# Kernel tuning notes

Measured on AMD Instinct MI355X. Metric: run time of the kernel, lower is better.

The kernel has to match this reference:

```python
import jax, jax.numpy as jnp
import numpy as np

N = 100000      # nodes
E = 3200000     # edges
IN_DIM = 128
HID = 128
OUT_DIM = 1
LAYERS = 8
ALPHA = 0.1
THETA = 0.5


def setup_inputs() -> dict:
    key = jax.random.key(0)
    ks = jax.random.split(key, 8)
    x = jax.random.normal(ks[0], (N, IN_DIM), dtype=jnp.float32)
    edge_index = jax.random.randint(ks[1], (2, E), 0, N, dtype=jnp.int64)
    edge_weight = jax.random.uniform(ks[2], (E,), dtype=jnp.float32)  # unused by original forward path
    W_in = jax.random.normal(ks[3], (IN_DIM, HID), dtype=jnp.float32) * 0.05
    b_in = jnp.zeros((HID,), dtype=jnp.float32)
    W_gcn = jax.random.normal(ks[4], (LAYERS, HID, HID), dtype=jnp.float32) * 0.05
    W_out = jax.random.normal(ks[5], (HID, OUT_DIM), dtype=jnp.float32) * 0.05
    b_out = jnp.zeros((OUT_DIM,), dtype=jnp.float32)
    return {"x": x, "edge_weight": edge_weight, "W_in": W_in, "b_in": b_in,
            "W_gcn": W_gcn, "W_out": W_out, "b_out": b_out, "edge_index": edge_index}


def _gcn_norm(edge_index, dtype):
    # add self loops (fill value 1), symmetric normalization deg^-1/2 A deg^-1/2
    sl = jnp.arange(N, dtype=edge_index.dtype)
    row = jnp.concatenate([edge_index[0], sl])
    col = jnp.concatenate([edge_index[1], sl])
    w = jnp.ones(row.shape[0], dtype=dtype)
    deg = jax.ops.segment_sum(w, col, num_segments=N)
    dinv = jnp.where(deg > 0, jax.lax.rsqrt(deg), 0.0)
    norm = dinv[row] * dinv[col]
    return row, col, norm


def reference(x, edge_weight, W_in, b_in, W_gcn, W_out, b_out, edge_index):
    row, col, norm = _gcn_norm(edge_index, x.dtype)
    h = x @ W_in + b_in            # initial_proj
    h0 = h                          # residual x0
    for i in range(LAYERS):
        # dropout is identity in eval mode
        msg = h[row] * norm[:, None]                       # gather + scale [E+N, HID]
        agg = jax.ops.segment_sum(msg, col, num_segments=N)
        s = (1.0 - ALPHA) * agg + ALPHA * h0               # identity-mapped residual
        beta = float(np.log(THETA / (i + 1) + 1.0))
        h = (1.0 - beta) * s + beta * (s @ W_gcn[i])       # GCNII weight mix
        h = jax.nn.relu(h)
    return h @ W_out + b_out
```

## Files before the change

### kernel.cpp

```cpp
#include <hip/hip_runtime.h>
#include <hip/hip_bf16.h>
#include <math.h>

#define N_NODES 100000
#define N_EDGES 3200000
#define HID 128
#define LAYERS 8
#define ALPHA 0.1f
#define THETA 0.5f

#define NBKT 391
#define BKT_STRIDE 10240
#define EPT 16
#define CHUNK 4096

typedef unsigned int uint;
typedef unsigned short ushort;
typedef __attribute__((ext_vector_type(8))) short short8;
typedef __attribute__((ext_vector_type(4))) float f32x4;

__device__ inline float bf_lo(uint p) { return __uint_as_float(p << 16); }
__device__ inline float bf_hi(uint p) { return __uint_as_float(p & 0xffff0000u); }
__device__ inline uint bf_pack(float x, float y) {
    uint ux = __float_as_uint(x), uy = __float_as_uint(y);
    uint rx = (ux + 0x7fffu + ((ux >> 16) & 1u)) >> 16;
    uint ry = (uy + 0x7fffu + ((uy >> 16) & 1u)) >> 16;
    return rx | (ry << 16);
}
__device__ inline ushort bfr(float x) {
    uint u = __float_as_uint(x);
    return (ushort)((u + 0x7fffu + ((u >> 16) & 1u)) >> 16);
}
__device__ inline float bff(ushort s) { return __uint_as_float(((uint)s) << 16); }

__global__ __launch_bounds__(256) void k_bucket(const int* __restrict__ rowi,
                                                const int* __restrict__ coli,
                                                uint* __restrict__ eb,
                                                int* __restrict__ gcnt) {
    __shared__ int bcnt[NBKT];
    __shared__ int gbase[NBKT];
    int t = threadIdx.x;
    for (int i = t; i < NBKT; i += 256) bcnt[i] = 0;
    __syncthreads();

    int e0 = blockIdx.x * CHUNK;
    int bk[EPT];
    int rk[EPT];
    uint rec[EPT];
#pragma unroll
    for (int j = 0; j < EPT; ++j) {
        int e = e0 + j * 256 + t;
        if (e < N_EDGES) {
            int r = rowi[e];
            int c = coli[e];
            bk[j] = c >> 8;
            rec[j] = ((uint)r << 8) | (uint)(c & 255);
            rk[j] = atomicAdd(&bcnt[bk[j]], 1);
        } else {
            bk[j] = -1;
        }
    }
    __syncthreads();
    for (int i = t; i < NBKT; i += 256) {
        int n = bcnt[i];
        gbase[i] = n ? atomicAdd(&gcnt[i], n) : 0;
    }
    __syncthreads();
#pragma unroll
    for (int j = 0; j < EPT; ++j) {
        if (bk[j] >= 0)
            eb[(size_t)bk[j] * BKT_STRIDE + gbase[bk[j]] + rk[j]] = rec[j];
    }
}

__global__ __launch_bounds__(512) void k_bscan(const int* __restrict__ gcnt,
                                               int* __restrict__ bbase) {
    __shared__ int lds[512];
    int t = threadIdx.x;
    int v = (t < NBKT) ? gcnt[t] : 0;
    lds[t] = v;
    __syncthreads();
    for (int off = 1; off < 512; off <<= 1) {
        int u = (t >= off) ? lds[t - off] : 0;
        __syncthreads();
        lds[t] += u;
        __syncthreads();
    }
    if (t < NBKT) bbase[t] = lds[t] - v;
}

__global__ __launch_bounds__(256) void k_node_ipt(const uint* __restrict__ eb,
                                                  const int* __restrict__ gcnt,
                                                  const int* __restrict__ bbase,
                                                  float* __restrict__ dinv,
                                                  int* __restrict__ indptr) {
    __shared__ int ncnt[256];
    __shared__ int sc[256];
    int b = blockIdx.x;
    int t = threadIdx.x;
    ncnt[t] = 0;
    __syncthreads();
    int ne = gcnt[b];
    const uint* ebp = eb + (size_t)b * BKT_STRIDE;
    for (int i = t; i < ne; i += 256) atomicAdd(&ncnt[ebp[i] & 255], 1);
    __syncthreads();
    int v = ncnt[t];
    sc[t] = v;
    __syncthreads();
    for (int off = 1; off < 256; off <<= 1) {
        int u = (t >= off) ? sc[t - off] : 0;
        __syncthreads();
        sc[t] += u;
        __syncthreads();
    }
    int node = b * 256 + t;
    if (node < N_NODES) {
        dinv[node] = rsqrtf((float)(v + 1));
        indptr[node] = bbase[b] + (sc[t] - v);
    }
    if (b == NBKT - 1 && t == 255) indptr[N_NODES] = N_EDGES;
}

__global__ __launch_bounds__(256) void k_fill2(const uint* __restrict__ eb,
                                               const int* __restrict__ gcnt,
                                               const float* __restrict__ dinv,
                                               const int* __restrict__ indptr,
                                               int2* __restrict__ csr) {
    __shared__ float sdv[256];
    __shared__ int scur[256];
    __shared__ int sipt[256];
    int b = blockIdx.x;
    int t = threadIdx.x;
    int node = b * 256 + t;
    sdv[t] = (node < N_NODES) ? dinv[node] : 0.f;
    sipt[t] = (node < N_NODES) ? indptr[node] : 0;
    scur[t] = 0;
    __syncthreads();
    int ne = gcnt[b];
    const uint* ebp = eb + (size_t)b * BKT_STRIDE;
    for (int i = t; i < ne; i += 256) {
        uint rec = ebp[i];
        int lc = rec & 255;
        int r = (int)(rec >> 8);
        int pos = sipt[lc] + atomicAdd(&scur[lc], 1);
        csr[pos] = make_int2(r, __float_as_int(dinv[r] * sdv[lc]));
    }
}

__global__ __launch_bounds__(256) void k_wprep(const float* __restrict__ Wg,
                                               ushort* __restrict__ Wt) {
    int l = blockIdx.x;
    const float* W = Wg + (size_t)l * HID * HID;
    ushort* T = Wt + (size_t)l * HID * HID;
    int t = threadIdx.x;
#pragma unroll
    for (int i = 0; i < 16; ++i) {
        int idx = t + 256 * i;
        int k = idx >> 5;
        int c4 = idx & 31;
        float4 v = *(const float4*)(W + (size_t)k * HID + c4 * 4);
        T[(c4 * 4 + 0) * HID + k] = bfr(v.x);
        T[(c4 * 4 + 1) * HID + k] = bfr(v.y);
        T[(c4 * 4 + 2) * HID + k] = bfr(v.z);
        T[(c4 * 4 + 3) * HID + k] = bfr(v.w);
    }
}

__global__ __launch_bounds__(256) void k_spmm(const uint* __restrict__ h,
                                              const uint* __restrict__ h0,
                                              const float* __restrict__ dinv,
                                              const int* __restrict__ indptr,
                                              const int2* __restrict__ csr,
                                              uint* __restrict__ s_out) {
    int node = blockIdx.x * 4 + (threadIdx.x >> 6);
    if (node >= N_NODES) return;
    int lane = threadIdx.x & 63;
    int beg = indptr[node];
    int end = indptr[node + 1];
    float di = dinv[node];
    uint hs = h[node * 64 + lane];
    uint h0v = h0[node * 64 + lane];
    float ax[8], ay[8];
#pragma unroll
    for (int j = 0; j < 8; ++j) { ax[j] = 0.f; ay[j] = 0.f; }
    int e = beg;
    for (; e + 16 <= end; e += 16) {
        int2 rr[16];
#pragma unroll
        for (int j = 0; j < 16; ++j) rr[j] = csr[e + j];
        uint p[16];
#pragma unroll
        for (int j = 0; j < 16; ++j) p[j] = h[rr[j].x * 64 + lane];
#pragma unroll
        for (int j = 0; j < 16; ++j) {
            float w = __int_as_float(rr[j].y);
            ax[j & 7] = fmaf(w, bf_lo(p[j]), ax[j & 7]);
            ay[j & 7] = fmaf(w, bf_hi(p[j]), ay[j & 7]);
        }
    }
    for (; e < end; e += 4) {
        int2 rr[4];
        float w[4];
#pragma unroll
        for (int j = 0; j < 4; ++j) {
            int idx = e + j;
            rr[j] = csr[idx < end ? idx : beg];
            w[j] = (idx < end) ? __int_as_float(rr[j].y) : 0.f;
        }
        uint p[4];
#pragma unroll
        for (int j = 0; j < 4; ++j) p[j] = h[rr[j].x * 64 + lane];
#pragma unroll
        for (int j = 0; j < 4; ++j) {
            ax[j] = fmaf(w[j], bf_lo(p[j]), ax[j]);
            ay[j] = fmaf(w[j], bf_hi(p[j]), ay[j]);
        }
    }
    float sum0 = ((ax[0] + ax[1]) + (ax[2] + ax[3])) + ((ax[4] + ax[5]) + (ax[6] + ax[7]));
    float sum1 = ((ay[0] + ay[1]) + (ay[2] + ay[3])) + ((ay[4] + ay[5]) + (ay[6] + ay[7]));
    float selfw = di * di;
    float rx = (1.0f - ALPHA) * fmaf(selfw, bf_lo(hs), sum0) + ALPHA * bf_lo(h0v);
    float ry = (1.0f - ALPHA) * fmaf(selfw, bf_hi(hs), sum1) + ALPHA * bf_hi(h0v);
    s_out[node * 64 + lane] = bf_pack(rx, ry);
}

__global__ __launch_bounds__(256) void k_gemm_in(const float* __restrict__ A,
                                                 const float* __restrict__ W,
                                                 const float* __restrict__ bias,
                                                 uint* __restrict__ out0,
                                                 uint* __restrict__ out1) {
    __shared__ float sT[32 * 64];
    __shared__ float Ws[32 * 128];
    int t = threadIdx.x;
    int tr = t & 15;
    int tc = t >> 4;
    int rowBase = blockIdx.x * 64;
    float acc[4][8] = {};

    for (int ko = 0; ko < HID; ko += 32) {
#pragma unroll
        for (int pass = 0; pass < 2; ++pass) {
            int lin = t + 256 * pass;
            int r = lin >> 3;
            int kq = lin & 7;
            int ar = rowBase + r;
            if (ar >= N_NODES) ar = N_NODES - 1;
            float4 v = *(const float4*)(A + (size_t)ar * HID + ko + 4 * kq);
            sT[(4 * kq + 0) * 64 + r] = v.x;
            sT[(4 * kq + 1) * 64 + r] = v.y;
            sT[(4 * kq + 2) * 64 + r] = v.z;
            sT[(4 * kq + 3) * 64 + r] = v.w;
        }
#pragma unroll
        for (int pass = 0; pass < 4; ++pass) {
            int lin = t + 256 * pass;
            int k = lin >> 5;
            int c4 = lin & 31;
            *(float4*)&Ws[k * 128 + 4 * c4] =
                *(const float4*)(W + (size_t)(ko + k) * HID + 4 * c4);
        }
        __syncthreads();
#pragma unroll
        for (int k = 0; k < 32; ++k) {
            float4 a = *(const float4*)&sT[k * 64 + 4 * tr];
            float4 w0 = *(const float4*)&Ws[k * 128 + 8 * tc];
            float4 w1 = *(const float4*)&Ws[k * 128 + 8 * tc + 4];
            float av[4] = {a.x, a.y, a.z, a.w};
            float wv[8] = {w0.x, w0.y, w0.z, w0.w, w1.x, w1.y, w1.z, w1.w};
#pragma unroll
            for (int i = 0; i < 4; ++i)
#pragma unroll
                for (int j = 0; j < 8; ++j)
                    acc[i][j] = fmaf(av[i], wv[j], acc[i][j]);
        }
        __syncthreads();
    }

    int c0 = 8 * tc;
    float bb[8];
#pragma unroll
    for (int j = 0; j < 8; ++j) bb[j] = bias[c0 + j];
#pragma unroll
    for (int i = 0; i < 4; ++i) {
        int r = rowBase + 4 * tr + i;
        if (r >= N_NODES) break;
        float v[8];
#pragma unroll
        for (int j = 0; j < 8; ++j) v[j] = acc[i][j] + bb[j];
        uint4 o;
        o.x = bf_pack(v[0], v[1]);
        o.y = bf_pack(v[2], v[3]);
        o.z = bf_pack(v[4], v[5]);
        o.w = bf_pack(v[6], v[7]);
        *(uint4*)(out0 + (size_t)r * 64 + c0 / 2) = o;
        *(uint4*)(out1 + (size_t)r * 64 + c0 / 2) = o;
    }
}

#define SAS 136

__global__ __launch_bounds__(256) void k_gemm_layer(const uint* __restrict__ A,
                                                    const ushort* __restrict__ Wt,
                                                    uint* __restrict__ out0,
                                                    float beta) {
    __shared__ ushort sA[64 * SAS];
    __shared__ ushort sW[128 * SAS];
    int t = threadIdx.x;
    int lane = t & 63;
    int wv = t >> 6;
    int rowBase = blockIdx.x * 64;

#pragma unroll
    for (int i = 0; i < 4; ++i) {
        int idx = t + 256 * i;
        int r = idx >> 4;
        int q = idx & 15;
        int ar = rowBase + r;
        if (ar >= N_NODES) ar = N_NODES - 1;
        uint4 v = *(const uint4*)(A + (size_t)ar * 64 + q * 4);
        *(uint4*)((uint*)(sA + r * SAS) + q * 4) = v;
    }
#pragma unroll
    for (int i = 0; i < 8; ++i) {
        int idx = t + 256 * i;
        int r = idx >> 4;
        int q = idx & 15;
        uint4 v = *(const uint4*)((const uint*)(Wt + (size_t)r * HID) + q * 4);
        *(uint4*)((uint*)(sW + r * SAS) + q * 4) = v;
    }
    __syncthreads();

    int fr = lane & 15;
    int fq = lane >> 4;
    f32x4 acc[4][2] = {};
#pragma unroll
    for (int kc = 0; kc < 4; ++kc) {
        int kof = kc * 32 + fq * 8;
        short8 b0 = *(const short8*)(sW + (wv * 32 + fr) * SAS + kof);
        short8 b1 = *(const short8*)(sW + (wv * 32 + 16 + fr) * SAS + kof);
#pragma unroll
        for (int tm = 0; tm < 4; ++tm) {
            short8 a = *(const short8*)(sA + (tm * 16 + fr) * SAS + kof);
            acc[tm][0] = __builtin_amdgcn_mfma_f32_16x16x32_bf16(a, b0, acc[tm][0], 0, 0, 0);
            acc[tm][1] = __builtin_amdgcn_mfma_f32_16x16x32_bf16(a, b1, acc[tm][1], 0, 0, 0);
        }
    }
    __syncthreads();

    ushort* pack = sW;
    float ob = 1.0f - beta;
#pragma unroll
    for (int tm = 0; tm < 4; ++tm)
#pragma unroll
        for (int tn = 0; tn < 2; ++tn)
#pragma unroll
            for (int r = 0; r < 4; ++r) {
                int row = tm * 16 + fq * 4 + r;
                int col = wv * 32 + tn * 16 + fr;
                float sv = bff(sA[row * SAS + col]);
                float val = fmaxf(fmaf(ob, sv, beta * acc[tm][tn][r]), 0.f);
                pack[row * 128 + col] = bfr(val);
            }
    __syncthreads();
#pragma unroll
    for (int i = 0; i < 4; ++i) {
        int idx = t + 256 * i;
        int r = idx >> 4;
        int q = idx & 15;
        int ar = rowBase + r;
        if (ar < N_NODES)
            *(uint4*)(out0 + (size_t)ar * 64 + q * 4) =
                *(const uint4*)((const uint*)(pack + r * 128) + q * 4);
    }
}

__global__ __launch_bounds__(256) void k_out(const uint* __restrict__ h,
                                             const float* __restrict__ W_out,
                                             const float* __restrict__ b_out,
                                             float* __restrict__ out) {
    int node = blockIdx.x * 4 + (threadIdx.x >> 6);
    if (node >= N_NODES) return;
    int lane = threadIdx.x & 63;
    uint p = h[node * 64 + lane];
    float2 wv = *(const float2*)(W_out + lane * 2);
    float pr = bf_lo(p) * wv.x + bf_hi(p) * wv.y;
#pragma unroll
    for (int off = 32; off > 0; off >>= 1) pr += __shfl_down(pr, off);
    if (lane == 0) out[node] = pr + b_out[0];
}

extern "C" void kernel_launch(void* const* d_in, const int* in_sizes, int n_in,
                              void* d_out, int out_size, void* d_ws, size_t ws_size,
                              hipStream_t stream) {
    const float* x     = (const float*)d_in[0];
    const float* W_in  = (const float*)d_in[2];
    const float* b_in  = (const float*)d_in[3];
    const float* W_gcn = (const float*)d_in[4];
    const float* W_out = (const float*)d_in[5];
    const float* b_out = (const float*)d_in[6];
    const int*   ei    = (const int*)d_in[7];
    const int* rowi = ei;
    const int* coli = ei + N_EDGES;
    float* out = (float*)d_out;

    char* ws = (char*)d_ws;
    auto alloc = [&](size_t bytes) -> char* {
        char* p = ws;
        ws += (bytes + 255) & ~(size_t)255;
        return p;
    };
    float*  dinv    = (float*) alloc((size_t)N_NODES * 4);
    int*    indptr  = (int*)   alloc((size_t)(N_NODES + 1) * 4);
    int*    gcnt    = (int*)   alloc(2048 * 4);
    int*    bbase   = (int*)   alloc(2048 * 4);
    int2*   csr     = (int2*)  alloc((size_t)N_EDGES * 8);
    ushort* Wt      = (ushort*)alloc((size_t)LAYERS * HID * HID * 2);
    uint*   hA      = (uint*)  alloc((size_t)N_NODES * 64 * 4);
    uint*   hB      = (uint*)  alloc((size_t)N_NODES * 64 * 4);
    uint*   h0      = (uint*)  alloc((size_t)N_NODES * 64 * 4);
    uint*   eb      = hB;

    hipMemsetAsync(gcnt, 0, (size_t)NBKT * 4, stream);

    k_bucket<<<(N_EDGES + CHUNK - 1) / CHUNK, 256, 0, stream>>>(rowi, coli, eb, gcnt);
    k_bscan<<<1, 512, 0, stream>>>(gcnt, bbase);
    k_node_ipt<<<NBKT, 256, 0, stream>>>(eb, gcnt, bbase, dinv, indptr);
    k_fill2<<<NBKT, 256, 0, stream>>>(eb, gcnt, dinv, indptr, csr);
    k_wprep<<<LAYERS, 256, 0, stream>>>(W_gcn, Wt);

    int gemm_blocks = (N_NODES + 63) / 64;
    k_gemm_in<<<gemm_blocks, 256, 0, stream>>>(x, W_in, b_in, h0, hA);

    for (int l = 0; l < LAYERS; ++l) {
        k_spmm<<<(N_NODES + 3) / 4, 256, 0, stream>>>(hA, h0, dinv, indptr,
                                                      csr, hB);
        float beta = logf(THETA / (float)(l + 1) + 1.0f);
        k_gemm_layer<<<gemm_blocks, 256, 0, stream>>>(
            hB, Wt + (size_t)l * HID * HID, hA, beta);
    }
    k_out<<<(N_NODES + 3) / 4, 256, 0, stream>>>(hA, W_out, b_out, out);
}
```

Before: 1.307 ms.

## Fuse SpMM aggregation and per-layer GEMM into one kernel

The separate sparse aggregation and dense layer GEMM kernels are merged into a single per-layer kernel. Each block aggregates 64 nodes into shared memory (16 nodes per wave, serially), then runs the MFMA GEMM directly from that buffer, reading weights straight from global memory instead of staging them in LDS. This removes the intermediate s buffer's write and read plus one launch per layer, and ping-pongs the h buffers. The cost is less parallelism per node in the gather phase, since each wave walks 16 nodes sequentially with fewer blocks in flight, which may hurt latency hiding for the random gathers.

```diff
diff --git a/kernel.cpp b/kernel.cpp
--- a/kernel.cpp
+++ b/kernel.cpp
@@ -164,64 +164,6 @@
         T[(c4 * 4 + 2) * HID + k] = bfr(v.z);
         T[(c4 * 4 + 3) * HID + k] = bfr(v.w);
     }
-}
-
-__global__ __launch_bounds__(256) void k_spmm(const uint* __restrict__ h,
-                                              const uint* __restrict__ h0,
-                                              const float* __restrict__ dinv,
-                                              const int* __restrict__ indptr,
-                                              const int2* __restrict__ csr,
-                                              uint* __restrict__ s_out) {
-    int node = blockIdx.x * 4 + (threadIdx.x >> 6);
-    if (node >= N_NODES) return;
-    int lane = threadIdx.x & 63;
-    int beg = indptr[node];
-    int end = indptr[node + 1];
-    float di = dinv[node];
-    uint hs = h[node * 64 + lane];
-    uint h0v = h0[node * 64 + lane];
-    float ax[8], ay[8];
-#pragma unroll
-    for (int j = 0; j < 8; ++j) { ax[j] = 0.f; ay[j] = 0.f; }
-    int e = beg;
-    for (; e + 16 <= end; e += 16) {
-        int2 rr[16];
-#pragma unroll
-        for (int j = 0; j < 16; ++j) rr[j] = csr[e + j];
-        uint p[16];
-#pragma unroll
-        for (int j = 0; j < 16; ++j) p[j] = h[rr[j].x * 64 + lane];
-#pragma unroll
-        for (int j = 0; j < 16; ++j) {
-            float w = __int_as_float(rr[j].y);
-            ax[j & 7] = fmaf(w, bf_lo(p[j]), ax[j & 7]);
-            ay[j & 7] = fmaf(w, bf_hi(p[j]), ay[j & 7]);
-        }
-    }
-    for (; e < end; e += 4) {
-        int2 rr[4];
-        float w[4];
-#pragma unroll
-        for (int j = 0; j < 4; ++j) {
-            int idx = e + j;
-            rr[j] = csr[idx < end ? idx : beg];
-            w[j] = (idx < end) ? __int_as_float(rr[j].y) : 0.f;
-        }
-        uint p[4];
-#pragma unroll
-        for (int j = 0; j < 4; ++j) p[j] = h[rr[j].x * 64 + lane];
-#pragma unroll
-        for (int j = 0; j < 4; ++j) {
-            ax[j] = fmaf(w[j], bf_lo(p[j]), ax[j]);
-            ay[j] = fmaf(w[j], bf_hi(p[j]), ay[j]);
-        }
-    }
-    float sum0 = ((ax[0] + ax[1]) + (ax[2] + ax[3])) + ((ax[4] + ax[5]) + (ax[6] + ax[7]));
-    float sum1 = ((ay[0] + ay[1]) + (ay[2] + ay[3])) + ((ay[4] + ay[5]) + (ay[6] + ay[7]));
-    float selfw = di * di;
-    float rx = (1.0f - ALPHA) * fmaf(selfw, bf_lo(hs), sum0) + ALPHA * bf_lo(h0v);
-    float ry = (1.0f - ALPHA) * fmaf(selfw, bf_hi(hs), sum1) + ALPHA * bf_hi(h0v);
-    s_out[node * 64 + lane] = bf_pack(rx, ry);
 }
 
 __global__ __launch_bounds__(256) void k_gemm_in(const float* __restrict__ A,
@@ -299,34 +241,76 @@
 
 #define SAS 136
 
-__global__ __launch_bounds__(256) void k_gemm_layer(const uint* __restrict__ A,
-                                                    const ushort* __restrict__ Wt,
-                                                    uint* __restrict__ out0,
-                                                    float beta) {
+__global__ __launch_bounds__(256) void k_layer(const uint* __restrict__ h,
+                                               const uint* __restrict__ h0,
+                                               const float* __restrict__ dinv,
+                                               const int* __restrict__ indptr,
+                                               const int2* __restrict__ csr,
+                                               const ushort* __restrict__ Wt,
+                                               uint* __restrict__ out0,
+                                               float beta) {
     __shared__ ushort sA[64 * SAS];
-    __shared__ ushort sW[128 * SAS];
+    __shared__ ushort pack[64 * 128];
     int t = threadIdx.x;
     int lane = t & 63;
     int wv = t >> 6;
     int rowBase = blockIdx.x * 64;
 
-#pragma unroll
-    for (int i = 0; i < 4; ++i) {
-        int idx = t + 256 * i;
-        int r = idx >> 4;
-        int q = idx & 15;
-        int ar = rowBase + r;
-        if (ar >= N_NODES) ar = N_NODES - 1;
-        uint4 v = *(const uint4*)(A + (size_t)ar * 64 + q * 4);
-        *(uint4*)((uint*)(sA + r * SAS) + q * 4) = v;
-    }
-#pragma unroll
-    for (int i = 0; i < 8; ++i) {
-        int idx = t + 256 * i;
-        int r = idx >> 4;
-        int q = idx & 15;
-        uint4 v = *(const uint4*)((const uint*)(Wt + (size_t)r * HID) + q * 4);
-        *(uint4*)((uint*)(sW + r * SAS) + q * 4) = v;
+#pragma unroll 1
+    for (int i = 0; i < 16; ++i) {
+        int r = wv * 16 + i;
+        int node = rowBase + r;
+        uint outv = 0;
+        if (node < N_NODES) {
+            int beg = indptr[node];
+            int end = indptr[node + 1];
+            float di = dinv[node];
+            uint hs = h[node * 64 + lane];
+            uint h0v = h0[node * 64 + lane];
+            float ax[8], ay[8];
+#pragma unroll
+            for (int j = 0; j < 8; ++j) { ax[j] = 0.f; ay[j] = 0.f; }
+            int e = beg;
+            for (; e + 16 <= end; e += 16) {
+                int2 rr[16];
+#pragma unroll
+                for (int j = 0; j < 16; ++j) rr[j] = csr[e + j];
+                uint p[16];
+#pragma unroll
+                for (int j = 0; j < 16; ++j) p[j] = h[rr[j].x * 64 + lane];
+#pragma unroll
+                for (int j = 0; j < 16; ++j) {
+                    float w = __int_as_float(rr[j].y);
+                    ax[j & 7] = fmaf(w, bf_lo(p[j]), ax[j & 7]);
+                    ay[j & 7] = fmaf(w, bf_hi(p[j]), ay[j & 7]);
+                }
+            }
+            for (; e < end; e += 4) {
+                int2 rr[4];
+                float w[4];
+#pragma unroll
+                for (int j = 0; j < 4; ++j) {
+                    int idx = e + j;
+                    rr[j] = csr[idx < end ? idx : beg];
+                    w[j] = (idx < end) ? __int_as_float(rr[j].y) : 0.f;
+                }
+                uint p[4];
+#pragma unroll
+                for (int j = 0; j < 4; ++j) p[j] = h[rr[j].x * 64 + lane];
+#pragma unroll
+                for (int j = 0; j < 4; ++j) {
+                    ax[j] = fmaf(w[j], bf_lo(p[j]), ax[j]);
+                    ay[j] = fmaf(w[j], bf_hi(p[j]), ay[j]);
+                }
+            }
+            float sum0 = ((ax[0] + ax[1]) + (ax[2] + ax[3])) + ((ax[4] + ax[5]) + (ax[6] + ax[7]));
+            float sum1 = ((ay[0] + ay[1]) + (ay[2] + ay[3])) + ((ay[4] + ay[5]) + (ay[6] + ay[7]));
+            float selfw = di * di;
+            float rx = (1.0f - ALPHA) * fmaf(selfw, bf_lo(hs), sum0) + ALPHA * bf_lo(h0v);
+            float ry = (1.0f - ALPHA) * fmaf(selfw, bf_hi(hs), sum1) + ALPHA * bf_hi(h0v);
+            outv = bf_pack(rx, ry);
+        }
+        ((uint*)(sA + r * SAS))[lane] = outv;
     }
     __syncthreads();
 
@@ -336,8 +320,8 @@
 #pragma unroll
     for (int kc = 0; kc < 4; ++kc) {
         int kof = kc * 32 + fq * 8;
-        short8 b0 = *(const short8*)(sW + (wv * 32 + fr) * SAS + kof);
-        short8 b1 = *(const short8*)(sW + (wv * 32 + 16 + fr) * SAS + kof);
+        short8 b0 = *(const short8*)(Wt + (size_t)(wv * 32 + fr) * HID + kof);
+        short8 b1 = *(const short8*)(Wt + (size_t)(wv * 32 + 16 + fr) * HID + kof);
 #pragma unroll
         for (int tm = 0; tm < 4; ++tm) {
             short8 a = *(const short8*)(sA + (tm * 16 + fr) * SAS + kof);
@@ -345,9 +329,7 @@
             acc[tm][1] = __builtin_amdgcn_mfma_f32_16x16x32_bf16(a, b1, acc[tm][1], 0, 0, 0);
         }
     }
-    __syncthreads();
-
-    ushort* pack = sW;
+
     float ob = 1.0f - beta;
 #pragma unroll
     for (int tm = 0; tm < 4; ++tm)
@@ -431,12 +413,14 @@
     int gemm_blocks = (N_NODES + 63) / 64;
     k_gemm_in<<<gemm_blocks, 256, 0, stream>>>(x, W_in, b_in, h0, hA);
 
+    uint* hin = hA;
+    uint* hout = hB;
     for (int l = 0; l < LAYERS; ++l) {
-        k_spmm<<<(N_NODES + 3) / 4, 256, 0, stream>>>(hA, h0, dinv, indptr,
-                                                      csr, hB);
         float beta = logf(THETA / (float)(l + 1) + 1.0f);
-        k_gemm_layer<<<gemm_blocks, 256, 0, stream>>>(
-            hB, Wt + (size_t)l * HID * HID, hA, beta);
-    }
-    k_out<<<(N_NODES + 3) / 4, 256, 0, stream>>>(hA, W_out, b_out, out);
-}
+        k_layer<<<gemm_blocks, 256, 0, stream>>>(hin, h0, dinv, indptr, csr,
+                                                 Wt + (size_t)l * HID * HID,
+                                                 hout, beta);
+        uint* tmp = hin; hin = hout; hout = tmp;
+    }
+    k_out<<<(N_NODES + 3) / 4, 256, 0, stream>>>(hin, W_out, b_out, out);
+}
```

Result: slower. 1.769 ms (+35.3%).

## Use half-wave per node in SpMM and read GEMM weights from global

Applied to the files above, without the earlier changes.

The SpMM kernel now assigns 32 lanes per node, each loading a uint2 (4 bf16 values), so every gathered row is fetched with wider 8-byte loads and 8 nodes fit per block. The unroll depth drops to 8 edges with two accumulator sets. The layer GEMM stops staging the weight matrix in shared memory and reads B fragments straight from global/L2, which removes the weight copy and a barrier and shrinks LDS use to raise occupancy. The trade-off is less memory-level parallelism per lane in the gather and uncoalesced repeated weight reads that depend on cache hits.

```diff
diff --git a/kernel.cpp b/kernel.cpp
--- a/kernel.cpp
+++ b/kernel.cpp
@@ -172,56 +172,67 @@
                                               const int* __restrict__ indptr,
                                               const int2* __restrict__ csr,
                                               uint* __restrict__ s_out) {
-    int node = blockIdx.x * 4 + (threadIdx.x >> 6);
+    int node = blockIdx.x * 8 + (threadIdx.x >> 5);
     if (node >= N_NODES) return;
-    int lane = threadIdx.x & 63;
+    int l = threadIdx.x & 31;
     int beg = indptr[node];
     int end = indptr[node + 1];
     float di = dinv[node];
-    uint hs = h[node * 64 + lane];
-    uint h0v = h0[node * 64 + lane];
-    float ax[8], ay[8];
-#pragma unroll
-    for (int j = 0; j < 8; ++j) { ax[j] = 0.f; ay[j] = 0.f; }
+    uint2 hs = *(const uint2*)(h + node * 64 + l * 2);
+    uint2 h0v = *(const uint2*)(h0 + node * 64 + l * 2);
+    float a0[2] = {0.f, 0.f}, a1[2] = {0.f, 0.f};
+    float a2[2] = {0.f, 0.f}, a3[2] = {0.f, 0.f};
     int e = beg;
-    for (; e + 16 <= end; e += 16) {
-        int2 rr[16];
-#pragma unroll
-        for (int j = 0; j < 16; ++j) rr[j] = csr[e + j];
-        uint p[16];
-#pragma unroll
-        for (int j = 0; j < 16; ++j) p[j] = h[rr[j].x * 64 + lane];
-#pragma unroll
-        for (int j = 0; j < 16; ++j) {
+    for (; e + 8 <= end; e += 8) {
+        int2 rr[8];
+#pragma unroll
+        for (int j = 0; j < 8; ++j) rr[j] = csr[e + j];
+        uint2 p[8];
+#pragma unroll
+        for (int j = 0; j < 8; ++j) p[j] = *(const uint2*)(h + rr[j].x * 64 + l * 2);
+#pragma unroll
+        for (int j = 0; j < 8; ++j) {
             float w = __int_as_float(rr[j].y);
-            ax[j & 7] = fmaf(w, bf_lo(p[j]), ax[j & 7]);
-            ay[j & 7] = fmaf(w, bf_hi(p[j]), ay[j & 7]);
-        }
-    }
-    for (; e < end; e += 4) {
-        int2 rr[4];
-        float w[4];
-#pragma unroll
-        for (int j = 0; j < 4; ++j) {
+            int d = j & 1;
+            a0[d] = fmaf(w, bf_lo(p[j].x), a0[d]);
+            a1[d] = fmaf(w, bf_hi(p[j].x), a1[d]);
+            a2[d] = fmaf(w, bf_lo(p[j].y), a2[d]);
+            a3[d] = fmaf(w, bf_hi(p[j].y), a3[d]);
+        }
+    }
+    for (; e < end; e += 2) {
+        int2 rr[2];
+        float w[2];
+#pragma unroll
+        for (int j = 0; j < 2; ++j) {
             int idx = e + j;
             rr[j] = csr[idx < end ? idx : beg];
             w[j] = (idx < end) ? __int_as_float(rr[j].y) : 0.f;
         }
-        uint p[4];
-#pragma unroll
-        for (int j = 0; j < 4; ++j) p[j] = h[rr[j].x * 64 + lane];
-#pragma unroll
-        for (int j = 0; j < 4; ++j) {
-            ax[j] = fmaf(w[j], bf_lo(p[j]), ax[j]);
-            ay[j] = fmaf(w[j], bf_hi(p[j]), ay[j]);
-        }
-    }
-    float sum0 = ((ax[0] + ax[1]) + (ax[2] + ax[3])) + ((ax[4] + ax[5]) + (ax[6] + ax[7]));
-    float sum1 = ((ay[0] + ay[1]) + (ay[2] + ay[3])) + ((ay[4] + ay[5]) + (ay[6] + ay[7]));
+        uint2 p[2];
+#pragma unroll
+        for (int j = 0; j < 2; ++j) p[j] = *(const uint2*)(h + rr[j].x * 64 + l * 2);
+#pragma unroll
+        for (int j = 0; j < 2; ++j) {
+            a0[j] = fmaf(w[j], bf_lo(p[j].x), a0[j]);
+            a1[j] = fmaf(w[j], bf_hi(p[j].x), a1[j]);
+            a2[j] = fmaf(w[j], bf_lo(p[j].y), a2[j]);
+            a3[j] = fmaf(w[j], bf_hi(p[j].y), a3[j]);
+        }
+    }
+    float s0 = a0[0] + a0[1];
+    float s1 = a1[0] + a1[1];
+    float s2 = a2[0] + a2[1];
+    float s3 = a3[0] + a3[1];
     float selfw = di * di;
-    float rx = (1.0f - ALPHA) * fmaf(selfw, bf_lo(hs), sum0) + ALPHA * bf_lo(h0v);
-    float ry = (1.0f - ALPHA) * fmaf(selfw, bf_hi(hs), sum1) + ALPHA * bf_hi(h0v);
-    s_out[node * 64 + lane] = bf_pack(rx, ry);
+    float rx = (1.0f - ALPHA) * fmaf(selfw, bf_lo(hs.x), s0) + ALPHA * bf_lo(h0v.x);
+    float ry = (1.0f - ALPHA) * fmaf(selfw, bf_hi(hs.x), s1) + ALPHA * bf_hi(h0v.x);
+    float rz = (1.0f - ALPHA) * fmaf(selfw, bf_lo(hs.y), s2) + ALPHA * bf_lo(h0v.y);
+    float rw = (1.0f - ALPHA) * fmaf(selfw, bf_hi(hs.y), s3) + ALPHA * bf_hi(h0v.y);
+    uint2 o;
+    o.x = bf_pack(rx, ry);
+    o.y = bf_pack(rz, rw);
+    *(uint2*)(s_out + node * 64 + l * 2) = o;
 }
 
 __global__ __launch_bounds__(256) void k_gemm_in(const float* __restrict__ A,
@@ -304,7 +315,7 @@
                                                     uint* __restrict__ out0,
                                                     float beta) {
     __shared__ ushort sA[64 * SAS];
-    __shared__ ushort sW[128 * SAS];
+    __shared__ ushort pack[64 * 128];
     int t = threadIdx.x;
     int lane = t & 63;
     int wv = t >> 6;
@@ -320,24 +331,18 @@
         uint4 v = *(const uint4*)(A + (size_t)ar * 64 + q * 4);
         *(uint4*)((uint*)(sA + r * SAS) + q * 4) = v;
     }
-#pragma unroll
-    for (int i = 0; i < 8; ++i) {
-        int idx = t + 256 * i;
-        int r = idx >> 4;
-        int q = idx & 15;
-        uint4 v = *(const uint4*)((const uint*)(Wt + (size_t)r * HID) + q * 4);
-        *(uint4*)((uint*)(sW + r * SAS) + q * 4) = v;
-    }
     __syncthreads();
 
     int fr = lane & 15;
     int fq = lane >> 4;
+    const ushort* Wb0 = Wt + (size_t)(wv * 32 + fr) * HID;
+    const ushort* Wb1 = Wt + (size_t)(wv * 32 + 16 + fr) * HID;
     f32x4 acc[4][2] = {};
 #pragma unroll
     for (int kc = 0; kc < 4; ++kc) {
         int kof = kc * 32 + fq * 8;
-        short8 b0 = *(const short8*)(sW + (wv * 32 + fr) * SAS + kof);
-        short8 b1 = *(const short8*)(sW + (wv * 32 + 16 + fr) * SAS + kof);
+        short8 b0 = *(const short8*)(Wb0 + kof);
+        short8 b1 = *(const short8*)(Wb1 + kof);
 #pragma unroll
         for (int tm = 0; tm < 4; ++tm) {
             short8 a = *(const short8*)(sA + (tm * 16 + fr) * SAS + kof);
@@ -345,9 +350,7 @@
             acc[tm][1] = __builtin_amdgcn_mfma_f32_16x16x32_bf16(a, b1, acc[tm][1], 0, 0, 0);
         }
     }
-    __syncthreads();
-
-    ushort* pack = sW;
+
     float ob = 1.0f - beta;
 #pragma unroll
     for (int tm = 0; tm < 4; ++tm)
@@ -431,12 +434,14 @@
     int gemm_blocks = (N_NODES + 63) / 64;
     k_gemm_in<<<gemm_blocks, 256, 0, stream>>>(x, W_in, b_in, h0, hA);
 
+    uint* hin = hA;
+    uint* hout = hB;
     for (int l = 0; l < LAYERS; ++l) {
-        k_spmm<<<(N_NODES + 3) / 4, 256, 0, stream>>>(hA, h0, dinv, indptr,
-                                                      csr, hB);
+        k_spmm<<<(N_NODES + 7) / 8, 256, 0, stream>>>(hin, h0, dinv, indptr,
+                                                      csr, hout);
         float beta = logf(THETA / (float)(l + 1) + 1.0f);
         k_gemm_layer<<<gemm_blocks, 256, 0, stream>>>(
-            hB, Wt + (size_t)l * HID * HID, hA, beta);
-    }
-    k_out<<<(N_NODES + 3) / 4, 256, 0, stream>>>(hA, W_out, b_out, out);
-}
+            hout, Wt + (size_t)l * HID * HID, hin, beta);
+    }
+    k_out<<<(N_NODES + 3) / 4, 256, 0, stream>>>(hin, W_out, b_out, out);
+}
```

After: 1.352 ms. +3.5%, slower.
